# Kernel optimization log

Measured on AMD Instinct MI355X. Metric: run time of the kernel, lower is better.

Reference implementation:

```python
import jax, jax.numpy as jnp
import numpy as np

THRESHOLD = 0.0  # default float threshold, non-learned path
SURROGATE_TAU = 0.1

@jax.custom_vjp
def jumprelu(x):
    # Forward: hard threshold x * 1[x > THRESHOLD]
    return x * (x > THRESHOLD).astype(x.dtype)

def _jumprelu_fwd(x):
    return jumprelu(x), x

def _jumprelu_bwd(x, g):
    # Smooth surrogate gradient of x * sigmoid(x/tau)
    tau = SURROGATE_TAU
    sig = jax.nn.sigmoid(x / tau)
    surrogate = sig + x * sig * (1.0 - sig) / tau
    return (g * surrogate,)

jumprelu.defvjp(_jumprelu_fwd, _jumprelu_bwd)

NUM_TRANSFORMS = 64
D_MODEL = 2048
RANK = 32
BATCH = 2048

def setup_inputs() -> dict:
    key = jax.random.key(0)
    kx, kv, ku, ke = jax.random.split(key, 4)
    scale = (1.0 / (D_MODEL * RANK)) ** 0.25
    x = jax.random.normal(kx, (BATCH, D_MODEL), dtype=jnp.float32)
    V = jax.random.normal(kv, (NUM_TRANSFORMS, RANK, D_MODEL), dtype=jnp.float32) * scale
    U = jax.random.normal(ku, (NUM_TRANSFORMS, D_MODEL, RANK), dtype=jnp.float32) * scale
    encoder = jax.random.normal(ke, (NUM_TRANSFORMS, D_MODEL), dtype=jnp.float32)
    encoder = encoder / jnp.linalg.norm(encoder, axis=1, keepdims=True)
    bias = jnp.full((NUM_TRANSFORMS,), -1.0, dtype=jnp.float32)
    return {"x": x, "V": V, "U": U, "encoder": encoder, "bias": bias}

def reference(x, V, U, encoder, bias):
    # pre_acts: (batch, num_transforms)
    pre_acts = x @ encoder.T - bias
    gate = jumprelu(pre_acts)
    # Vx: (n, b, r); UVx: (n, b, d)
    Vx = jnp.einsum('nrd,bd->nbr', V, x)
    UVx = jnp.einsum('ndr,nbr->nbd', U, Vx)
    gated = UVx * gate.T[:, :, None]
    output = gated.sum(axis=0)  # (batch, d_model)
    u_norms = jnp.linalg.norm(U.reshape(U.shape[0], -1), axis=1)
    v_norms = jnp.linalg.norm(V.reshape(V.shape[0], -1), axis=1)
    frobenius_norms = u_norms * v_norms / (D_MODEL * RANK) ** 0.5
    return (output, gate, frobenius_norms)
```

## Files before the change

### kernel.cpp

```cpp
#include <hip/hip_runtime.h>


#define D_MODEL 2048
#define BATCH   2048
#define NT      64
#define RANK    32

typedef __attribute__((ext_vector_type(8))) __bf16 bf16x8;
typedef __attribute__((ext_vector_type(4))) float  f32x4;
typedef __attribute__((ext_vector_type(8))) unsigned short ushort8;

__device__ __forceinline__ unsigned short f2bf(float f) {
  unsigned int u = __builtin_bit_cast(unsigned int, f);
  u += 0x7FFFu + ((u >> 16) & 1u);
  return (unsigned short)(u >> 16);
}

__device__ __forceinline__ void gload_lds16(const void* g, void* l) {
  __builtin_amdgcn_global_load_lds(
      (const __attribute__((address_space(1))) unsigned int*)g,
      (__attribute__((address_space(3))) unsigned int*)l,
      16, 0, 0);
}

template <int N>
__device__ __forceinline__ void vm_wait_barrier() {
  if constexpr (N == 0)
    asm volatile("s_waitcnt vmcnt(0)\ns_barrier" ::: "memory");
  else if constexpr (N == 8)
    asm volatile("s_waitcnt vmcnt(8)\ns_barrier" ::: "memory");
  else if constexpr (N == 9)
    asm volatile("s_waitcnt vmcnt(9)\ns_barrier" ::: "memory");
  else
    static_assert(N == 0 || N == 8 || N == 9, "add vmcnt case");
}


__device__ __forceinline__ void block_reduce_store(float ss, float* dst, int slot) {
  __shared__ float red[256];
  int t = threadIdx.x;
  red[t] = ss;
  __syncthreads();
  for (int s = 128; s > 0; s >>= 1) {
    if (t < s) red[t] += red[t + s];
    __syncthreads();
  }
  if (t == 0) dst[slot] = red[0];
}

__global__ void k_prep(const float4* __restrict__ x, const float4* __restrict__ enc,
                       const float4* __restrict__ V, const float4* __restrict__ U,
                       ushort4* __restrict__ xb, ushort4* __restrict__ encb,
                       ushort4* __restrict__ Vb, unsigned short* __restrict__ Ut,
                       float* __restrict__ partV, float* __restrict__ partU) {
  int bid = blockIdx.x, t = threadIdx.x;
  if (bid < 1024) {
#pragma unroll
    for (int it = 0; it < 4; ++it) {
      int i = bid * 1024 + it * 256 + t;
      float4 v = x[i];
      ushort4 o;
      o.x = f2bf(v.x); o.y = f2bf(v.y); o.z = f2bf(v.z); o.w = f2bf(v.w);
      xb[i] = o;
    }
  } else if (bid < 1152) {
    int i = (bid - 1024) * 256 + t;
    float4 v = enc[i];
    ushort4 o;
    o.x = f2bf(v.x); o.y = f2bf(v.y); o.z = f2bf(v.z); o.w = f2bf(v.w);
    encb[i] = o;
  } else if (bid < 1408) {
    int b = bid - 1152;
    size_t base4 = (size_t)b * 4096;
    float ss = 0.f;
    for (int it = 0; it < 16; ++it) {
      size_t idx = base4 + t + it * 256;
      float4 v = V[idx];
      ss += v.x * v.x + v.y * v.y + v.z * v.z + v.w * v.w;
      ushort4 o;
      o.x = f2bf(v.x); o.y = f2bf(v.y); o.z = f2bf(v.z); o.w = f2bf(v.w);
      Vb[idx] = o;
    }
    block_reduce_store(ss, partV, b);
  } else {
    int b = bid - 1408;
    int n = b >> 2;
    size_t base4 = (size_t)b * 4096;
    float ss = 0.f;
    for (int it = 0; it < 8; ++it) {
      size_t i2 = (size_t)(it * 256 + t) * 2;
      size_t idx4 = base4 + i2;
      float4 v0 = U[idx4];
      float4 v1 = U[idx4 + 1];
      ss += v0.x * v0.x + v0.y * v0.y + v0.z * v0.z + v0.w * v0.w;
      ss += v1.x * v1.x + v1.y * v1.y + v1.z * v1.z + v1.w * v1.w;
      size_t e = idx4 * 4 - (size_t)n * (D_MODEL * RANK);
      int dcol = (int)(e >> 5);
      int r = (int)(e & 31);
      ushort8 o;
      o[0] = f2bf(v0.x); o[1] = f2bf(v0.y); o[2] = f2bf(v0.z); o[3] = f2bf(v0.w);
      o[4] = f2bf(v1.x); o[5] = f2bf(v1.y); o[6] = f2bf(v1.z); o[7] = f2bf(v1.w);
      *(ushort8*)(Ut + (size_t)dcol * 2048 + n * 32 + r) = o;
    }
    block_reduce_store(ss, partU, b);
  }
}

template <int WGM, int WGN, int MI, int NJ, int EPI, int SWZ>
__global__ __launch_bounds__(WGM * WGN * 64, 2)
void gemm_bt(const unsigned short* __restrict__ A,
             const unsigned short* __restrict__ Bt,
             unsigned short* __restrict__ outB,
             float* __restrict__ outF, int K, int klen,
             const unsigned short* __restrict__ Eb,
             const float* __restrict__ bias,
             const float* __restrict__ pU, const float* __restrict__ pV,
             float* __restrict__ frob, float* __restrict__ gateOut) {
  constexpr int VW = WGM * WGN;
  constexpr int BM = WGM * MI * 16;
  constexpr int BN = WGN * NJ * 16;
  constexpr int BK = 128;
  constexpr int GA = BM / (4 * VW);
  constexpr int GB = BN / (4 * VW);
  constexpr int LPW = GA + GB + (EPI == 0 ? 1 : 0);
  constexpr int HBUF = (BM + BN) * BK;
  constexpr int ENCS = (EPI == 0) ? 512 : 0;
  static_assert(EPI != 0 || (WGM == 2 && WGN == 4 && MI == 4 && NJ == 2),
                "EPI0 fused-gate layout requires 2x4 waves, MI=4, NJ=2");
  __shared__ __align__(16) unsigned short smem[2 * HBUF + 2 * ENCS];

  const int tid = threadIdx.x;
  const int w = tid >> 6;
  const int lane = tid & 63;
  const int quad = lane >> 4;
  const int l15 = lane & 15;
  const int wm = w % WGM;
  const int wn = w / WGM;

  int blockM, blockN;
  if constexpr (SWZ) {
    const int lin = blockIdx.x;
    const int xcd = lin & 7;
    const int i = lin >> 3;
    blockM = (xcd & 3) * 4 + (i & 3);
    blockN = (xcd >> 2) * 8 + (i >> 2);
  } else {
    blockN = blockIdx.x;
    blockM = blockIdx.y;
  }

  if constexpr (EPI == 0) {
    if (blockIdx.x == 0 && tid < NT) {
      float su = pU[4 * tid] + pU[4 * tid + 1] + pU[4 * tid + 2] + pU[4 * tid + 3];
      float sv = pV[4 * tid] + pV[4 * tid + 1] + pV[4 * tid + 2] + pV[4 * tid + 3];
      frob[tid] = sqrtf(su) * sqrtf(sv) * (1.0f / 256.0f);
    }
  }

  const int lrow4 = lane >> 4;
  const int key = ((w & 3) << 2) | lrow4;
  const int lq = l15 ^ key;
  const unsigned short* Ag = A + (size_t)(blockM * BM + w * 4 + lrow4) * K + lq * 8;
  const unsigned short* Bg = Bt + (size_t)(blockN * BN + w * 4 + lrow4) * K + lq * 8;
  const unsigned short* Eg = (EPI == 0)
      ? Eb + (size_t)(blockN * 4 + lrow4) * K + l15 * 8 : nullptr;

  const int rfA = wm * MI * 16 + l15;
  const int rfB = wn * NJ * 16 + l15;

  f32x4 acc[MI][NJ];
  f32x4 acc_g[MI];
  const f32x4 z = {0.f, 0.f, 0.f, 0.f};
#pragma unroll
  for (int i = 0; i < MI; ++i) {
    acc_g[i] = z;
#pragma unroll
    for (int j = 0; j < NJ; ++j) acc[i][j] = z;
  }

  auto stage = [&](int buf, int k0) {
    unsigned short* As = smem + buf * HBUF;
    unsigned short* Bs = As + BM * BK;
#pragma unroll
    for (int j = 0; j < GA; ++j)
      gload_lds16(Ag + (size_t)(j * VW * 4) * K + k0,
                  (char*)As + (j * VW + w) * 1024);
#pragma unroll
    for (int j = 0; j < GB; ++j)
      gload_lds16(Bg + (size_t)(j * VW * 4) * K + k0,
                  (char*)Bs + (j * VW + w) * 1024);
    if constexpr (EPI == 0)
      gload_lds16(Eg + k0, (char*)(smem + 2 * HBUF + buf * ENCS));
  };

  stage(0, 0);

  const int nt = klen / BK;
  int cur = 0;
  for (int t = 0; t < nt; ++t) {
    if (t + 1 < nt) {
      stage(cur ^ 1, (t + 1) * BK);
      vm_wait_barrier<LPW>();
    } else {
      vm_wait_barrier<0>();
    }
    const unsigned short* As = smem + cur * HBUF;
    const unsigned short* Bs = As + BM * BK;
    const unsigned short* Es = smem + 2 * HBUF + cur * ENCS;
#pragma unroll
    for (int s = 0; s < 4; ++s) {
      bf16x8 af[MI], bfr[NJ];
#pragma unroll
      for (int i = 0; i < MI; ++i)
        af[i] = *(const bf16x8*)((const char*)As + (rfA + i * 16) * 256 +
                                 (((s * 4 + quad) ^ l15) << 4));
#pragma unroll
      for (int j = 0; j < NJ; ++j)
        bfr[j] = *(const bf16x8*)((const char*)Bs + (rfB + j * 16) * 256 +
                                  (((s * 4 + quad) ^ l15) << 4));
      if constexpr (EPI == 0) {
        if (s == wn) {
          bf16x8 be = *(const bf16x8*)((const char*)Es +
                                       ((l15 & 3) * 128 + s * 32 + quad * 8) * 2);
#pragma unroll
          for (int i = 0; i < MI; ++i)
            acc_g[i] = __builtin_amdgcn_mfma_f32_16x16x32_bf16(af[i], be, acc_g[i], 0, 0, 0);
        }
      }
#pragma unroll
      for (int i = 0; i < MI; ++i)
#pragma unroll
        for (int j = 0; j < NJ; ++j)
          acc[i][j] = __builtin_amdgcn_mfma_f32_16x16x32_bf16(af[i], bfr[j], acc[i][j], 0, 0, 0);
    }
    asm volatile("s_barrier" ::: "memory");
    cur ^= 1;
  }

  const int row0 = blockM * BM + wm * MI * 16 + quad * 4;
  const int col0 = blockN * BN + wn * NJ * 16 + l15;
  if constexpr (EPI == 0) {
    float* tmp = (float*)smem;
    if (l15 < 4) {
#pragma unroll
      for (int i = 0; i < MI; ++i)
#pragma unroll
        for (int r = 0; r < 4; ++r)
          tmp[(((wn * 2 + wm) * MI + i) * 16 + quad * 4 + r) * 4 + l15] = acc_g[i][r];
    }
    __syncthreads();
    const float bv = bias[blockN * 4 + wn];
#pragma unroll
    for (int i = 0; i < MI; ++i) {
#pragma unroll
      for (int t = 0; t < 4; ++t) {
        float s0 = tmp[(((0 * 2 + wm) * MI + i) * 16 + quad * 4 + t) * 4 + wn]
                 + tmp[(((1 * 2 + wm) * MI + i) * 16 + quad * 4 + t) * 4 + wn]
                 + tmp[(((2 * 2 + wm) * MI + i) * 16 + quad * 4 + t) * 4 + wn]
                 + tmp[(((3 * 2 + wm) * MI + i) * 16 + quad * 4 + t) * 4 + wn];
        float pre = s0 - bv;
        float g = pre > 0.f ? pre : 0.f;
        const int row = row0 + i * 16 + t;
        if (l15 == 0)
          gateOut[(size_t)row * NT + blockN * 4 + wn] = g;
#pragma unroll
        for (int j = 0; j < NJ; ++j)
          outB[(size_t)row * 2048 + col0 + j * 16] = f2bf(acc[i][j][t] * g);
      }
    }
  } else {
#pragma unroll
    for (int i = 0; i < MI; ++i) {
#pragma unroll
      for (int j = 0; j < NJ; ++j) {
        const int col = col0 + j * 16;
#pragma unroll
        for (int t = 0; t < 4; ++t) {
          const int row = row0 + i * 16 + t;
          outF[(size_t)row * 2048 + col] = acc[i][j][t];
        }
      }
    }
  }
}


extern "C" void kernel_launch(void* const* d_in, const int* in_sizes, int n_in,
                              void* d_out, int out_size, void* d_ws, size_t ws_size,
                              hipStream_t stream) {
  const float* x    = (const float*)d_in[0];
  const float* V    = (const float*)d_in[1];
  const float* U    = (const float*)d_in[2];
  const float* enc  = (const float*)d_in[3];
  const float* bias = (const float*)d_in[4];

  float* out  = (float*)d_out;
  float* gate = out + (size_t)BATCH * D_MODEL;
  float* frob = gate + (size_t)BATCH * NT;

  char* ws = (char*)d_ws;
  unsigned short* xb   = (unsigned short*)(ws);
  unsigned short* Vb   = (unsigned short*)(ws + (8u << 20));
  unsigned short* Ut   = (unsigned short*)(ws + (16u << 20));
  unsigned short* Yg   = (unsigned short*)(ws + (24u << 20));
  unsigned short* encb = (unsigned short*)(ws + (32u << 20));
  float* partU = (float*)(ws + (32u << 20) + 262144);
  float* partV = partU + 256;

  k_prep<<<1664, 256, 0, stream>>>((const float4*)x, (const float4*)enc,
                                   (const float4*)V, (const float4*)U,
                                   (ushort4*)xb, (ushort4*)encb, (ushort4*)Vb, Ut,
                                   partV, partU);

  gemm_bt<2, 4, 4, 2, 0, 1><<<dim3(256, 1, 1), 512, 0, stream>>>(
      xb, Vb, Yg, nullptr, D_MODEL, D_MODEL,
      encb, bias, partU, partV, frob, gate);

  gemm_bt<2, 4, 4, 2, 1, 1><<<dim3(256, 1, 1), 512, 0, stream>>>(
      Yg, Ut, nullptr, out, D_MODEL, D_MODEL,
      nullptr, nullptr, nullptr, nullptr, nullptr, nullptr);
}
```

Measured before the change: 145.5 us.

## Fuse prep and both GEMMs into one cooperative kernel with grid syncs

Replaces the three separate launches (bf16 conversion/norm prep, gated first GEMM, second GEMM) with one cooperative persistent kernel of 256 blocks. The phases are separated by threadfence plus grid.sync. The prep work is redistributed across the 256 blocks, and the GEMM bodies become device functions with constant sizes. This removes kernel launch gaps and tail effects between stages. In exchange it adds the cost of grid-wide barriers, and it needs all 256 blocks to be co-resident.

After: 314.0 us. 116% more time.

```diff
diff --git a/kernel.cpp b/kernel.cpp
--- a/kernel.cpp
+++ b/kernel.cpp
@@ -1,4 +1,7 @@
 #include <hip/hip_runtime.h>
+#include <hip/hip_cooperative_groups.h>
+
+namespace cg = cooperative_groups;
 
 
 #define D_MODEL 2048
@@ -35,101 +38,26 @@
     static_assert(N == 0 || N == 8 || N == 9, "add vmcnt case");
 }
 
-
-__device__ __forceinline__ void block_reduce_store(float ss, float* dst, int slot) {
-  __shared__ float red[256];
-  int t = threadIdx.x;
-  red[t] = ss;
-  __syncthreads();
-  for (int s = 128; s > 0; s >>= 1) {
-    if (t < s) red[t] += red[t + s];
-    __syncthreads();
-  }
-  if (t == 0) dst[slot] = red[0];
-}
-
-__global__ void k_prep(const float4* __restrict__ x, const float4* __restrict__ enc,
-                       const float4* __restrict__ V, const float4* __restrict__ U,
-                       ushort4* __restrict__ xb, ushort4* __restrict__ encb,
-                       ushort4* __restrict__ Vb, unsigned short* __restrict__ Ut,
-                       float* __restrict__ partV, float* __restrict__ partU) {
-  int bid = blockIdx.x, t = threadIdx.x;
-  if (bid < 1024) {
-#pragma unroll
-    for (int it = 0; it < 4; ++it) {
-      int i = bid * 1024 + it * 256 + t;
-      float4 v = x[i];
-      ushort4 o;
-      o.x = f2bf(v.x); o.y = f2bf(v.y); o.z = f2bf(v.z); o.w = f2bf(v.w);
-      xb[i] = o;
-    }
-  } else if (bid < 1152) {
-    int i = (bid - 1024) * 256 + t;
-    float4 v = enc[i];
-    ushort4 o;
-    o.x = f2bf(v.x); o.y = f2bf(v.y); o.z = f2bf(v.z); o.w = f2bf(v.w);
-    encb[i] = o;
-  } else if (bid < 1408) {
-    int b = bid - 1152;
-    size_t base4 = (size_t)b * 4096;
-    float ss = 0.f;
-    for (int it = 0; it < 16; ++it) {
-      size_t idx = base4 + t + it * 256;
-      float4 v = V[idx];
-      ss += v.x * v.x + v.y * v.y + v.z * v.z + v.w * v.w;
-      ushort4 o;
-      o.x = f2bf(v.x); o.y = f2bf(v.y); o.z = f2bf(v.z); o.w = f2bf(v.w);
-      Vb[idx] = o;
-    }
-    block_reduce_store(ss, partV, b);
-  } else {
-    int b = bid - 1408;
-    int n = b >> 2;
-    size_t base4 = (size_t)b * 4096;
-    float ss = 0.f;
-    for (int it = 0; it < 8; ++it) {
-      size_t i2 = (size_t)(it * 256 + t) * 2;
-      size_t idx4 = base4 + i2;
-      float4 v0 = U[idx4];
-      float4 v1 = U[idx4 + 1];
-      ss += v0.x * v0.x + v0.y * v0.y + v0.z * v0.z + v0.w * v0.w;
-      ss += v1.x * v1.x + v1.y * v1.y + v1.z * v1.z + v1.w * v1.w;
-      size_t e = idx4 * 4 - (size_t)n * (D_MODEL * RANK);
-      int dcol = (int)(e >> 5);
-      int r = (int)(e & 31);
-      ushort8 o;
-      o[0] = f2bf(v0.x); o[1] = f2bf(v0.y); o[2] = f2bf(v0.z); o[3] = f2bf(v0.w);
-      o[4] = f2bf(v1.x); o[5] = f2bf(v1.y); o[6] = f2bf(v1.z); o[7] = f2bf(v1.w);
-      *(ushort8*)(Ut + (size_t)dcol * 2048 + n * 32 + r) = o;
-    }
-    block_reduce_store(ss, partU, b);
-  }
-}
-
-template <int WGM, int WGN, int MI, int NJ, int EPI, int SWZ>
-__global__ __launch_bounds__(WGM * WGN * 64, 2)
-void gemm_bt(const unsigned short* __restrict__ A,
-             const unsigned short* __restrict__ Bt,
-             unsigned short* __restrict__ outB,
-             float* __restrict__ outF, int K, int klen,
-             const unsigned short* __restrict__ Eb,
-             const float* __restrict__ bias,
-             const float* __restrict__ pU, const float* __restrict__ pV,
-             float* __restrict__ frob, float* __restrict__ gateOut) {
+template <int EPI>
+__device__ __forceinline__ void gemm_body(
+    unsigned short* smem, const int bid, const int tid,
+    const unsigned short* __restrict__ A,
+    const unsigned short* __restrict__ Bt,
+    unsigned short* __restrict__ outB, float* __restrict__ outF,
+    const unsigned short* __restrict__ Eb,
+    const float* __restrict__ bias, float* __restrict__ gateOut) {
+  constexpr int WGM = 2, WGN = 4, MI = 4, NJ = 2;
   constexpr int VW = WGM * WGN;
   constexpr int BM = WGM * MI * 16;
   constexpr int BN = WGN * NJ * 16;
   constexpr int BK = 128;
+  constexpr int K = 2048;
   constexpr int GA = BM / (4 * VW);
   constexpr int GB = BN / (4 * VW);
   constexpr int LPW = GA + GB + (EPI == 0 ? 1 : 0);
   constexpr int HBUF = (BM + BN) * BK;
-  constexpr int ENCS = (EPI == 0) ? 512 : 0;
-  static_assert(EPI != 0 || (WGM == 2 && WGN == 4 && MI == 4 && NJ == 2),
-                "EPI0 fused-gate layout requires 2x4 waves, MI=4, NJ=2");
-  __shared__ __align__(16) unsigned short smem[2 * HBUF + 2 * ENCS];
-
-  const int tid = threadIdx.x;
+  constexpr int ENCS = 512;
+
   const int w = tid >> 6;
   const int lane = tid & 63;
   const int quad = lane >> 4;
@@ -137,25 +65,10 @@
   const int wm = w % WGM;
   const int wn = w / WGM;
 
-  int blockM, blockN;
-  if constexpr (SWZ) {
-    const int lin = blockIdx.x;
-    const int xcd = lin & 7;
-    const int i = lin >> 3;
-    blockM = (xcd & 3) * 4 + (i & 3);
-    blockN = (xcd >> 2) * 8 + (i >> 2);
-  } else {
-    blockN = blockIdx.x;
-    blockM = blockIdx.y;
-  }
-
-  if constexpr (EPI == 0) {
-    if (blockIdx.x == 0 && tid < NT) {
-      float su = pU[4 * tid] + pU[4 * tid + 1] + pU[4 * tid + 2] + pU[4 * tid + 3];
-      float sv = pV[4 * tid] + pV[4 * tid + 1] + pV[4 * tid + 2] + pV[4 * tid + 3];
-      frob[tid] = sqrtf(su) * sqrtf(sv) * (1.0f / 256.0f);
-    }
-  }
+  const int xcd = bid & 7;
+  const int i0 = bid >> 3;
+  const int blockM = (xcd & 3) * 4 + (i0 & 3);
+  const int blockN = (xcd >> 2) * 8 + (i0 >> 2);
 
   const int lrow4 = lane >> 4;
   const int key = ((w & 3) << 2) | lrow4;
@@ -195,7 +108,7 @@
 
   stage(0, 0);
 
-  const int nt = klen / BK;
+  constexpr int nt = 2048 / BK;
   int cur = 0;
   for (int t = 0; t < nt; ++t) {
     if (t + 1 < nt) {
@@ -284,39 +197,136 @@
   }
 }
 
+__global__ __launch_bounds__(512, 2) void k_mega(
+    const float4* __restrict__ x, const float4* __restrict__ enc,
+    const float4* __restrict__ V, const float4* __restrict__ U,
+    const float* __restrict__ bias,
+    ushort4* __restrict__ xb, ushort4* __restrict__ encb,
+    ushort4* __restrict__ Vb, unsigned short* __restrict__ Ut,
+    unsigned short* __restrict__ Yg, float* __restrict__ out,
+    float* __restrict__ gate, float* __restrict__ frob,
+    float* __restrict__ partV, float* __restrict__ partU) {
+  constexpr int HBUF = 256 * 128;
+  constexpr int ENCS = 512;
+  __shared__ __align__(16) unsigned short smem[2 * HBUF + 2 * ENCS];
+
+  const int bid = blockIdx.x;
+  const int tid = threadIdx.x;
+  cg::grid_group grid = cg::this_grid();
+
+  {
+#pragma unroll
+    for (int it = 0; it < 8; ++it) {
+      int i = bid * 4096 + it * 512 + tid;
+      float4 v = x[i];
+      ushort4 o;
+      o.x = f2bf(v.x); o.y = f2bf(v.y); o.z = f2bf(v.z); o.w = f2bf(v.w);
+      xb[i] = o;
+    }
+    if (bid < 64) {
+      int i = bid * 512 + tid;
+      float4 v = enc[i];
+      ushort4 o;
+      o.x = f2bf(v.x); o.y = f2bf(v.y); o.z = f2bf(v.z); o.w = f2bf(v.w);
+      encb[i] = o;
+    }
+    float ssv = 0.f;
+#pragma unroll
+    for (int it = 0; it < 8; ++it) {
+      int i = bid * 4096 + it * 512 + tid;
+      float4 v = V[i];
+      ssv += v.x * v.x + v.y * v.y + v.z * v.z + v.w * v.w;
+      ushort4 o;
+      o.x = f2bf(v.x); o.y = f2bf(v.y); o.z = f2bf(v.z); o.w = f2bf(v.w);
+      Vb[i] = o;
+    }
+    float* red = (float*)smem;
+    red[tid] = ssv;
+    __syncthreads();
+    for (int s = 256; s > 0; s >>= 1) {
+      if (tid < s) red[tid] += red[tid + s];
+      __syncthreads();
+    }
+    if (tid == 0) partV[bid] = red[0];
+    __syncthreads();
+    const int n = bid >> 2;
+    const size_t base4 = (size_t)bid * 4096;
+    float ssu = 0.f;
+#pragma unroll
+    for (int it = 0; it < 4; ++it) {
+      size_t i2 = (size_t)(it * 512 + tid) * 2;
+      size_t idx4 = base4 + i2;
+      float4 v0 = U[idx4];
+      float4 v1 = U[idx4 + 1];
+      ssu += v0.x * v0.x + v0.y * v0.y + v0.z * v0.z + v0.w * v0.w;
+      ssu += v1.x * v1.x + v1.y * v1.y + v1.z * v1.z + v1.w * v1.w;
+      size_t e = ((size_t)(bid & 3) << 14) + (i2 << 2);
+      int dcol = (int)(e >> 5);
+      int r = (int)(e & 31);
+      ushort8 o;
+      o[0] = f2bf(v0.x); o[1] = f2bf(v0.y); o[2] = f2bf(v0.z); o[3] = f2bf(v0.w);
+      o[4] = f2bf(v1.x); o[5] = f2bf(v1.y); o[6] = f2bf(v1.z); o[7] = f2bf(v1.w);
+      *(ushort8*)(Ut + (size_t)dcol * 2048 + n * 32 + r) = o;
+    }
+    red[tid] = ssu;
+    __syncthreads();
+    for (int s = 256; s > 0; s >>= 1) {
+      if (tid < s) red[tid] += red[tid + s];
+      __syncthreads();
+    }
+    if (tid == 0) partU[bid] = red[0];
+    __syncthreads();
+  }
+
+  __threadfence();
+  grid.sync();
+
+  if (bid == 0 && tid < NT) {
+    float su = partU[4 * tid] + partU[4 * tid + 1] + partU[4 * tid + 2] + partU[4 * tid + 3];
+    float sv = partV[4 * tid] + partV[4 * tid + 1] + partV[4 * tid + 2] + partV[4 * tid + 3];
+    frob[tid] = sqrtf(su) * sqrtf(sv) * (1.0f / 256.0f);
+  }
+
+  gemm_body<0>(smem, bid, tid,
+               (const unsigned short*)xb, (const unsigned short*)Vb,
+               Yg, nullptr, (const unsigned short*)encb, bias, gate);
+
+  __threadfence();
+  grid.sync();
+
+  gemm_body<1>(smem, bid, tid,
+               Yg, Ut, nullptr, out, nullptr, nullptr, nullptr);
+}
+
 
 extern "C" void kernel_launch(void* const* d_in, const int* in_sizes, int n_in,
                               void* d_out, int out_size, void* d_ws, size_t ws_size,
                               hipStream_t stream) {
-  const float* x    = (const float*)d_in[0];
-  const float* V    = (const float*)d_in[1];
-  const float* U    = (const float*)d_in[2];
-  const float* enc  = (const float*)d_in[3];
-  const float* bias = (const float*)d_in[4];
+  const float4* x    = (const float4*)d_in[0];
+  const float4* V    = (const float4*)d_in[1];
+  const float4* U    = (const float4*)d_in[2];
+  const float4* enc  = (const float4*)d_in[3];
+  const float*  bias = (const float*)d_in[4];
 
   float* out  = (float*)d_out;
   float* gate = out + (size_t)BATCH * D_MODEL;
   float* frob = gate + (size_t)BATCH * NT;
 
   char* ws = (char*)d_ws;
-  unsigned short* xb   = (unsigned short*)(ws);
-  unsigned short* Vb   = (unsigned short*)(ws + (8u << 20));
+  ushort4* xb          = (ushort4*)(ws);
+  ushort4* Vb          = (ushort4*)(ws + (8u << 20));
   unsigned short* Ut   = (unsigned short*)(ws + (16u << 20));
   unsigned short* Yg   = (unsigned short*)(ws + (24u << 20));
-  unsigned short* encb = (unsigned short*)(ws + (32u << 20));
+  ushort4* encb        = (ushort4*)(ws + (32u << 20));
   float* partU = (float*)(ws + (32u << 20) + 262144);
   float* partV = partU + 256;
 
-  k_prep<<<1664, 256, 0, stream>>>((const float4*)x, (const float4*)enc,
-                                   (const float4*)V, (const float4*)U,
-                                   (ushort4*)xb, (ushort4*)encb, (ushort4*)Vb, Ut,
-                                   partV, partU);
-
-  gemm_bt<2, 4, 4, 2, 0, 1><<<dim3(256, 1, 1), 512, 0, stream>>>(
-      xb, Vb, Yg, nullptr, D_MODEL, D_MODEL,
-      encb, bias, partU, partV, frob, gate);
-
-  gemm_bt<2, 4, 4, 2, 1, 1><<<dim3(256, 1, 1), 512, 0, stream>>>(
-      Yg, Ut, nullptr, out, D_MODEL, D_MODEL,
-      nullptr, nullptr, nullptr, nullptr, nullptr, nullptr);
-}
+  void* args[] = {
+    (void*)&x, (void*)&enc, (void*)&V, (void*)&U, (void*)&bias,
+    (void*)&xb, (void*)&encb, (void*)&Vb, (void*)&Ut,
+    (void*)&Yg, (void*)&out, (void*)&gate, (void*)&frob,
+    (void*)&partV, (void*)&partU
+  };
+  hipLaunchCooperativeKernel((const void*)k_mega, dim3(256), dim3(512),
+                             args, 0, stream);
+}
```
